# Performance work log

Hardware: AMD Instinct MI355X
Metric: run time of the kernel (lower is better)

## Reference

```python
import jax, jax.numpy as jnp
import numpy as np

N = 100000
E = 1600000
GENE = 512
HID = 128
NCLS = 10
EPS = 1e-5  # BatchNorm1d default eps


def setup_inputs() -> dict:
    key = jax.random.key(0)
    ks = jax.random.split(key, 16)
    def lin(k, fan_in, fan_out):
        return (jax.random.normal(k, (fan_in, fan_out), jnp.float32) / np.sqrt(fan_in)).astype(jnp.float32)
    dims = [(GENE, HID), (HID, 2 * HID), (2 * HID, HID), (HID, HID // 2)]
    inp = {}
    inp["x"] = jax.random.normal(ks[0], (N, GENE), jnp.float32)
    inp["edge_index"] = jax.random.randint(ks[1], (2, E), 0, N)
    for i, (di, do) in enumerate(dims, start=1):
        inp[f"W{i}"] = lin(ks[1 + i], di, do)
        inp[f"b{i}"] = jnp.zeros((do,), jnp.float32)
        inp[f"g{i}"] = jnp.ones((do,), jnp.float32)     # BN gamma
        inp[f"beta{i}"] = jnp.zeros((do,), jnp.float32)  # BN beta
    inp["Wc"] = lin(ks[10], HID // 2, NCLS)
    inp["bc"] = jnp.zeros((NCLS,), jnp.float32)
    return inp


def gcn_conv(h_in, W, b, src, dst, deg_inv_sqrt):
    # PyG GCNConv: transform, then symmetric-normalized aggregation with self-loops
    h = h_in @ W                                   # [N, out]
    norm = (deg_inv_sqrt[src] * deg_inv_sqrt[dst])[:, None]  # [E, 1]
    agg = jnp.zeros_like(h).at[dst].add(h[src] * norm)       # scatter-add over edges
    agg = agg + h * (deg_inv_sqrt ** 2)[:, None]   # self-loop contribution (norm = 1/deg)
    return agg + b


def relu_bn(h, g, beta):
    # forward applies BatchNorm1d(F.relu(h)) in training mode (batch stats, biased var)
    h = jax.nn.relu(h)
    mu = h.mean(axis=0)
    var = h.var(axis=0)
    return (h - mu) * jax.lax.rsqrt(var + EPS) * g + beta


def reference(x, edge_index, W1, b1, g1, beta1, W2, b2, g2, beta2,
              W3, b3, g3, beta3, W4, b4, g4, beta4, Wc, bc):
    src, dst = edge_index[0], edge_index[1]
    # degree after adding self-loops (edge weight 1)
    deg = jnp.zeros((x.shape[0],), x.dtype).at[dst].add(1.0) + 1.0
    dis = jax.lax.rsqrt(deg)
    h = relu_bn(gcn_conv(x, W1, b1, src, dst, dis), g1, beta1)
    h = relu_bn(gcn_conv(h, W2, b2, src, dst, dis), g2, beta2)
    h = relu_bn(gcn_conv(h, W3, b3, src, dst, dis), g3, beta3)
    h = relu_bn(gcn_conv(h, W4, b4, src, dst, dis), g4, beta4)
    return h @ Wc + bc
```

## Files before the change

kernel.cpp:

```cpp
#include <hip/hip_runtime.h>
#include <hip/hip_bf16.h>

#define EPS_BN 1e-5f

using frag8 = __attribute__((ext_vector_type(8))) short;
using f32x4 = __attribute__((ext_vector_type(4))) float;

typedef const __attribute__((address_space(1))) void* gas_ptr;
typedef __attribute__((address_space(3))) void* las_ptr;

__device__ __forceinline__ void async_ld16(const void* g, void* l) {
  __builtin_amdgcn_global_load_lds((gas_ptr)g, (las_ptr)l, 16, 0, 0);
}

__device__ __forceinline__ float bfu2f(unsigned short u) {
  union { unsigned int i; float f; } c;
  c.i = (unsigned int)u << 16;
  return c.f;
}


__global__ void wtrans1_kernel(const float* __restrict__ W1, __hip_bfloat16* __restrict__ T) {
  int i = blockIdx.x * blockDim.x + threadIdx.x;
  if (i < 512 * 128) {
    int k = i / 128, f = i % 128;
    T[f * 512 + k] = __float2bfloat16(W1[i]);
  }
}

__global__ void scan1_kernel(const int* __restrict__ cnt, int* __restrict__ out,
                             int* __restrict__ bsum, float* __restrict__ dis, int n) {
  __shared__ int sdata[1024];
  int tid = threadIdx.x;
  int i = blockIdx.x * 1024 + tid;
  int v = (i < n) ? cnt[i] : 0;
  if (i < n) dis[i] = rsqrtf((float)v + 1.0f);
  sdata[tid] = v;
  __syncthreads();
  for (int off = 1; off < 1024; off <<= 1) {
    int t = (tid >= off) ? sdata[tid - off] : 0;
    __syncthreads();
    sdata[tid] += t;
    __syncthreads();
  }
  if (i < n) out[i] = sdata[tid] - v;
  if (tid == 1023) bsum[blockIdx.x] = sdata[1023];
}

__global__ void scan2_kernel(int* __restrict__ bsum, int nb) {
  __shared__ int sdata[1024];
  int tid = threadIdx.x;
  int v = (tid < nb) ? bsum[tid] : 0;
  sdata[tid] = v;
  __syncthreads();
  for (int off = 1; off < 1024; off <<= 1) {
    int t = (tid >= off) ? sdata[tid - off] : 0;
    __syncthreads();
    sdata[tid] += t;
    __syncthreads();
  }
  if (tid < nb) bsum[tid] = sdata[tid] - v;
}

__global__ void scan3_kernel(int* __restrict__ out, const int* __restrict__ bsum,
                             int n, int E) {
  int i = blockIdx.x * 1024 + threadIdx.x;
  if (i < n) out[i] += bsum[blockIdx.x];
  if (i == 0) out[n] = E;
}

template <int TN, int ASTAGE, int OMODE>
__device__ __forceinline__ void gemm_body(
    const void* __restrict__ Ap, const __hip_bfloat16* __restrict__ Bt,
    __hip_bfloat16* __restrict__ C, const float* __restrict__ bias,
    const float* __restrict__ rowscale,
    const float* __restrict__ statsIn, const float* __restrict__ g,
    const float* __restrict__ beta, float* __restrict__ statsOut, float invN,
    int Nr, int K, int F, int bx, int by) {
  constexpr int WM = (TN == 128) ? 64 : 32;
  constexpr int MI = WM / 16;
  constexpr int BPASS = TN / 64;
  __shared__ __align__(16) __hip_bfloat16 As[2][128 * 32];
  __shared__ __align__(16) __hip_bfloat16 Bs[2][TN * 32];
  __shared__ float sacc[128], sqc[128];
  __shared__ float ssc[256], ssb[256];
  int tid = (int)threadIdx.x;
  int wid = tid >> 6, lane = tid & 63;
  int rowBase = bx * 128;
  int colBase = by * TN;
  int wr, wc;
  if (TN == 128) { wr = (wid >> 1) * 64; wc = (wid & 1) * 64; }
  else           { wr = wid * 32;        wc = 0; }

  f32x4 zero = {0.f, 0.f, 0.f, 0.f};
  f32x4 acc[MI][4];
#pragma unroll
  for (int i = 0; i < MI; ++i)
#pragma unroll
    for (int j = 0; j < 4; ++j) acc[i][j] = zero;

  int lm = lane & 15;
  int k8 = (lane >> 4) * 8;

  int arow[2], alrow[2], akq[2], adst[2];
#pragma unroll
  for (int p = 0; p < 2; ++p) {
    int sidx = p * 256 + tid;
    alrow[p] = sidx >> 2;
    akq[p] = (sidx & 3) * 8;
    int gr = rowBase + alrow[p];
    if (gr >= Nr) gr = Nr - 1;
    arow[p] = gr;
    adst[p] = (p * 256 + wid * 64) * 16;
  }
  int bcol[BPASS], bkq[BPASS], bdst[BPASS];
#pragma unroll
  for (int p = 0; p < BPASS; ++p) {
    int sidx = p * 256 + tid;
    bcol[p] = colBase + (sidx >> 2);
    bkq[p] = (sidx & 3) * 8;
    bdst[p] = (p * 256 + wid * 64) * 16;
  }

  if constexpr (OMODE == 3) {
    if (tid < 128) { sacc[tid] = 0.f; sqc[tid] = 0.f; }
  }
  if constexpr (ASTAGE == 2) {
    for (int k = tid; k < K; k += 256) {
      float mean = statsIn[k] * invN;
      float var = statsIn[256 + k] * invN - mean * mean;
      float sc = g[k] * rsqrtf(var + EPS_BN);
      ssc[k] = sc;
      ssb[k] = beta[k] - mean * sc;
    }
    __syncthreads();
  }

  auto cvt_store_f32 = [&](int p, int buf, float4 a, float4 b2) {
    union { frag8 f; __hip_bfloat16 h[8]; } pk;
    pk.h[0] = __float2bfloat16(a.x);  pk.h[1] = __float2bfloat16(a.y);
    pk.h[2] = __float2bfloat16(a.z);  pk.h[3] = __float2bfloat16(a.w);
    pk.h[4] = __float2bfloat16(b2.x); pk.h[5] = __float2bfloat16(b2.y);
    pk.h[6] = __float2bfloat16(b2.z); pk.h[7] = __float2bfloat16(b2.w);
    *(frag8*)&As[buf][alrow[p] * 32 + akq[p]] = pk.f;
  };
  auto cvt_store_bn = [&](int p, int buf, int kk, ushort4 a, ushort4 b2) {
    union { frag8 f; __hip_bfloat16 h[8]; } pk;
    pk.h[0] = __float2bfloat16(bfu2f(a.x)  * ssc[kk + 0] + ssb[kk + 0]);
    pk.h[1] = __float2bfloat16(bfu2f(a.y)  * ssc[kk + 1] + ssb[kk + 1]);
    pk.h[2] = __float2bfloat16(bfu2f(a.z)  * ssc[kk + 2] + ssb[kk + 2]);
    pk.h[3] = __float2bfloat16(bfu2f(a.w)  * ssc[kk + 3] + ssb[kk + 3]);
    pk.h[4] = __float2bfloat16(bfu2f(b2.x) * ssc[kk + 4] + ssb[kk + 4]);
    pk.h[5] = __float2bfloat16(bfu2f(b2.y) * ssc[kk + 5] + ssb[kk + 5]);
    pk.h[6] = __float2bfloat16(bfu2f(b2.z) * ssc[kk + 6] + ssb[kk + 6]);
    pk.h[7] = __float2bfloat16(bfu2f(b2.w) * ssc[kk + 7] + ssb[kk + 7]);
    *(frag8*)&As[buf][alrow[p] * 32 + akq[p]] = pk.f;
  };

  if constexpr (ASTAGE == 0) {
#pragma unroll
    for (int p = 0; p < 2; ++p)
      async_ld16((const __hip_bfloat16*)Ap + (size_t)arow[p] * K + akq[p],
                 (char*)As[0] + adst[p]);
  } else if constexpr (ASTAGE == 1) {
#pragma unroll
    for (int p = 0; p < 2; ++p) {
      const float* s = (const float*)Ap + (size_t)arow[p] * K + akq[p];
      cvt_store_f32(p, 0, *(const float4*)s, *(const float4*)(s + 4));
    }
  } else {
#pragma unroll
    for (int p = 0; p < 2; ++p) {
      const unsigned short* s = (const unsigned short*)Ap + (size_t)arow[p] * K + akq[p];
      cvt_store_bn(p, 0, akq[p], *(const ushort4*)s, *(const ushort4*)(s + 4));
    }
  }
#pragma unroll
  for (int p = 0; p < BPASS; ++p)
    async_ld16(Bt + (size_t)bcol[p] * K + bkq[p], (char*)Bs[0] + bdst[p]);
  __syncthreads();

  int nt = K >> 5;
  int cur = 0;
  for (int t = 0; t < nt; ++t) {
    int k0n = (t + 1) << 5;
    bool hasNext = (t + 1) < nt;
    float4 pf0[2], pf1[2];
    ushort4 pu0[2], pu1[2];

    if (hasNext) {
      if constexpr (ASTAGE == 0) {
#pragma unroll
        for (int p = 0; p < 2; ++p)
          async_ld16((const __hip_bfloat16*)Ap + (size_t)arow[p] * K + k0n + akq[p],
                     (char*)As[cur ^ 1] + adst[p]);
      } else if constexpr (ASTAGE == 1) {
#pragma unroll
        for (int p = 0; p < 2; ++p) {
          const float* s = (const float*)Ap + (size_t)arow[p] * K + k0n + akq[p];
          pf0[p] = *(const float4*)s;
          pf1[p] = *(const float4*)(s + 4);
        }
      } else {
#pragma unroll
        for (int p = 0; p < 2; ++p) {
          const unsigned short* s =
              (const unsigned short*)Ap + (size_t)arow[p] * K + k0n + akq[p];
          pu0[p] = *(const ushort4*)s;
          pu1[p] = *(const ushort4*)(s + 4);
        }
      }
#pragma unroll
      for (int p = 0; p < BPASS; ++p)
        async_ld16(Bt + (size_t)bcol[p] * K + k0n + bkq[p], (char*)Bs[cur ^ 1] + bdst[p]);
    }

    frag8 af[MI], bfr[4];
#pragma unroll
    for (int i = 0; i < MI; ++i)
      af[i] = *(const frag8*)&As[cur][(wr + i * 16 + lm) * 32 + k8];
#pragma unroll
    for (int j = 0; j < 4; ++j)
      bfr[j] = *(const frag8*)&Bs[cur][(wc + j * 16 + lm) * 32 + k8];
#pragma unroll
    for (int i = 0; i < MI; ++i)
#pragma unroll
      for (int j = 0; j < 4; ++j)
        acc[i][j] = __builtin_amdgcn_mfma_f32_16x16x32_bf16(af[i], bfr[j], acc[i][j], 0, 0, 0);

    if (hasNext) {
      if constexpr (ASTAGE == 1) {
#pragma unroll
        for (int p = 0; p < 2; ++p) cvt_store_f32(p, cur ^ 1, pf0[p], pf1[p]);
      } else if constexpr (ASTAGE == 2) {
#pragma unroll
        for (int p = 0; p < 2; ++p) cvt_store_bn(p, cur ^ 1, k0n + akq[p], pu0[p], pu1[p]);
      }
    }
    __syncthreads();
    cur ^= 1;
  }

  int rquad = (lane >> 4) * 4;
  float s[4] = {0.f, 0.f, 0.f, 0.f}, q[4] = {0.f, 0.f, 0.f, 0.f};
#pragma unroll
  for (int i = 0; i < MI; ++i) {
    int rb = rowBase + wr + i * 16 + rquad;
#pragma unroll
    for (int r = 0; r < 4; ++r) {
      int row = rb + r;
      if (row < Nr) {
        if constexpr (OMODE == 0) {
#pragma unroll
          for (int j = 0; j < 4; ++j) {
            int col = colBase + wc + j * 16 + lm;
            C[(size_t)row * F + col] = __float2bfloat16(acc[i][j][r]);
          }
        } else if constexpr (OMODE == 1) {
          float rs = rowscale[row];
#pragma unroll
          for (int j = 0; j < 4; ++j) {
            int col = colBase + wc + j * 16 + lm;
            C[(size_t)row * F + col] = __float2bfloat16(acc[i][j][r] * rs);
          }
        } else {
#pragma unroll
          for (int j = 0; j < 4; ++j) {
            int col = colBase + wc + j * 16 + lm;
            float v = acc[i][j][r] + bias[col];
            float rl = fmaxf(v, 0.f);
            C[(size_t)row * F + col] = __float2bfloat16(rl);
            s[j] += rl;
            q[j] += rl * rl;
          }
        }
      }
    }
  }

  if constexpr (OMODE == 3) {
#pragma unroll
    for (int j = 0; j < 4; ++j) {
      s[j] += __shfl_xor(s[j], 16, 64); s[j] += __shfl_xor(s[j], 32, 64);
      q[j] += __shfl_xor(q[j], 16, 64); q[j] += __shfl_xor(q[j], 32, 64);
    }
    if (lane < 16) {
#pragma unroll
      for (int j = 0; j < 4; ++j) {
        atomicAdd(&sacc[wc + j * 16 + lane], s[j]);
        atomicAdd(&sqc[wc + j * 16 + lane], q[j]);
      }
    }
    __syncthreads();
    if (tid < 128) {
      atomicAdd(&statsOut[colBase + tid], sacc[tid]);
      atomicAdd(&statsOut[256 + colBase + tid], sqc[tid]);
    }
  }
}

__global__ __launch_bounds__(256) void fat1_kernel(
    const float* __restrict__ x, const __hip_bfloat16* __restrict__ Wt0,
    __hip_bfloat16* __restrict__ T1, int Nn, int G1, int S,
    const int* __restrict__ e_dst, int* __restrict__ cnt, int* __restrict__ rank,
    int E, int CB,
    const float* __restrict__ W2, const float* __restrict__ W3, const float* __restrict__ W4,
    __hip_bfloat16* __restrict__ Tw2, __hip_bfloat16* __restrict__ Tw3,
    __hip_bfloat16* __restrict__ Tw4) {
  int b = (int)blockIdx.x;
  int inter = G1 * S;
  bool isGemm = (b < inter) && (b % S == 0);
  if (isGemm) {
    gemm_body<128, 1, 0>(x, Wt0, T1, nullptr, nullptr, nullptr, nullptr, nullptr,
                         nullptr, 0.f, Nn, 512, 128, b / S, 0);
    return;
  }
  int c = (b < inter) ? (b - b / S - 1) : (b - G1);
  if (c < CB) {
    int e = c * 256 + (int)threadIdx.x;
    if (e < E) rank[e] = atomicAdd(&cnt[e_dst[e]], 1);
  } else {
    int i = (c - CB) * 256 + (int)threadIdx.x;
    const float* W; __hip_bfloat16* T; int K, F, base;
    if (i < 32768)       { W = W2; T = Tw2; K = 128; F = 256; base = 0; }
    else if (i < 65536)  { W = W3; T = Tw3; K = 256; F = 128; base = 32768; }
    else if (i < 73728)  { W = W4; T = Tw4; K = 128; F = 64;  base = 65536; }
    else return;
    int j = i - base;
    int k = j / F, f = j % F;
    T[f * K + k] = __float2bfloat16(W[j]);
  }
}

template <int TN, int ASTAGE, int OMODE>
__global__ __launch_bounds__(256) void mfma_gemm_kernel(
    const void* __restrict__ A, const __hip_bfloat16* __restrict__ Bt,
    __hip_bfloat16* __restrict__ C, const float* __restrict__ bias,
    const float* __restrict__ rowscale, const float* __restrict__ statsIn,
    const float* __restrict__ g, const float* __restrict__ beta,
    float* __restrict__ statsOut, float invN, int Nr, int K, int F) {
  gemm_body<TN, ASTAGE, OMODE>(A, Bt, C, bias, rowscale, statsIn, g, beta, statsOut,
                               invN, Nr, K, F, (int)blockIdx.x, (int)blockIdx.y);
}

__global__ __launch_bounds__(256) void fat2_kernel(
    const int* __restrict__ src, const int* __restrict__ dst,
    const int* __restrict__ rowstart, const int* __restrict__ rank,
    int* __restrict__ csr_src, int E) {
  int e = (int)blockIdx.x * 256 + (int)threadIdx.x;
  if (e < E) csr_src[rowstart[dst[e]] + rank[e]] = src[e];
}

template <int VEC, int AMODE>
__global__ __launch_bounds__(256) void agg_kernel(
    const __hip_bfloat16* __restrict__ Ts, const int* __restrict__ rowstart,
    const int* __restrict__ csr_src, const float* __restrict__ dis,
    const float* __restrict__ bias, void* __restrict__ H,
    float* __restrict__ stats, const float* __restrict__ statsIn,
    const float* __restrict__ g, const float* __restrict__ beta,
    float* __restrict__ sd, float invN, int Nn, int F) {
  __shared__ float lsum[512], lqs[512];
  __shared__ float ssc[128], ssb[128];
  int tid = (int)threadIdx.x;
  int wid4 = tid >> 6;
  int lane = tid & 63;
  int off = lane * VEC;
  const unsigned short* Tu = (const unsigned short*)Ts;

  if constexpr (AMODE == 2) {
    if (tid < F) {
      float mean = statsIn[tid] * invN;
      float var = statsIn[256 + tid] * invN - mean * mean;
      float sc = g[tid] * rsqrtf(var + EPS_BN);
      ssc[tid] = sc;
      ssb[tid] = beta[tid] - mean * sc;
    }
    __syncthreads();
  }

  float bj[VEC];
  float s[VEC], q[VEC];
#pragma unroll
  for (int j = 0; j < VEC; ++j) {
    bj[j] = (AMODE == 1 || AMODE == 3 || AMODE == 4) ? bias[off + j] : 0.f;
    s[j] = 0.f; q[j] = 0.f;
  }

  for (int d = blockIdx.x * 4 + wid4; d < Nn; d += gridDim.x * 4) {
    float dd = dis[d];
    float acc[VEC];
    {
      unsigned short r[VEC];
      if constexpr (VEC == 2) *(ushort2*)r = *(const ushort2*)&Tu[(size_t)d * F + off];
      else                    r[0] = Tu[(size_t)d * F + off];
#pragma unroll
      for (int j = 0; j < VEC; ++j) {
        if constexpr (AMODE == 1) acc[j] = bfu2f(r[j]) * dd;
        else                      acc[j] = bfu2f(r[j]);
      }
    }
    float sdacc = dd;

    int e0 = rowstart[d], e1 = rowstart[d + 1];
    for (int e = e0; e < e1; e += 16) {
      int ee = e + (lane & 15);
      if (ee >= e1) ee = e1 - 1;
      int myidx = csr_src[ee];
      float mydis = 0.f;
      if constexpr (AMODE == 1) mydis = dis[myidx];
      int np = e1 - e;
      if (np > 16) np = 16;
      int sidx[16];
      float sdv[16];
#pragma unroll
      for (int p = 0; p < 16; ++p) {
        sidx[p] = __builtin_amdgcn_readlane(myidx, p);
        if constexpr (AMODE == 1)
          sdv[p] = __uint_as_float(
              (unsigned)__builtin_amdgcn_readlane((int)__float_as_uint(mydis), p));
      }
      unsigned short r[16][VEC];
#pragma unroll
      for (int p = 0; p < 16; ++p) {
        if constexpr (VEC == 2) *(ushort2*)r[p] = *(const ushort2*)&Tu[(size_t)sidx[p] * F + off];
        else                    r[p][0] = Tu[(size_t)sidx[p] * F + off];
      }
#pragma unroll
      for (int p = 0; p < 16; ++p) {
        if (p < np) {
          if constexpr (AMODE == 1) {
#pragma unroll
            for (int j = 0; j < VEC; ++j) acc[j] += bfu2f(r[p][j]) * sdv[p];
            sdacc += sdv[p];
          } else {
#pragma unroll
            for (int j = 0; j < VEC; ++j) acc[j] += bfu2f(r[p][j]);
          }
        }
      }
    }

    if constexpr (AMODE == 2) {
      float sdv = sd[d];
      union { ushort2 u; __hip_bfloat16 h[2]; } pk;
      pk.h[0] = __float2bfloat16(dd * (ssc[off + 0] * acc[0] + ssb[off + 0] * sdv));
      pk.h[1] = __float2bfloat16(dd * (ssc[off + 1] * acc[1] + ssb[off + 1] * sdv));
      *(ushort2*)&((__hip_bfloat16*)H)[(size_t)d * F + off] = pk.u;
    } else {
      float rl[VEC];
#pragma unroll
      for (int j = 0; j < VEC; ++j) {
        float v = acc[j] * dd + bj[j];
        rl[j] = fmaxf(v, 0.f);
        s[j] += rl[j];
        q[j] += rl[j] * rl[j];
      }
      if constexpr (AMODE == 1) {
        union { ushort2 u; __hip_bfloat16 h[2]; } pk;
        pk.h[0] = __float2bfloat16(rl[0] * dd);
        pk.h[1] = __float2bfloat16(rl[1] * dd);
        *(ushort2*)&((__hip_bfloat16*)H)[(size_t)d * F + off] = pk.u;
        if (lane == 0) sd[d] = sdacc;
      } else if constexpr (AMODE == 3) {
        union { ushort2 u; __hip_bfloat16 h[2]; } pk;
        pk.h[0] = __float2bfloat16(rl[0]);
        pk.h[1] = __float2bfloat16(rl[1]);
        *(ushort2*)&((__hip_bfloat16*)H)[(size_t)d * F + off] = pk.u;
      } else {
        ((float*)H)[(size_t)d * F + off] = rl[0];
      }
    }
  }

  if constexpr (AMODE != 2) {
#pragma unroll
    for (int j = 0; j < VEC; ++j) {
      lsum[(lane * VEC + j) * 4 + wid4] = s[j];
      lqs[(lane * VEC + j) * 4 + wid4] = q[j];
    }
    __syncthreads();
    int nc = 64 * VEC;
    for (int c = tid; c < nc; c += 256) {
      float a = lsum[c * 4 + 0] + lsum[c * 4 + 1] + lsum[c * 4 + 2] + lsum[c * 4 + 3];
      float b = lqs[c * 4 + 0] + lqs[c * 4 + 1] + lqs[c * 4 + 2] + lqs[c * 4 + 3];
      atomicAdd(&stats[c], a);
      atomicAdd(&stats[256 + c], b);
    }
  }
}

__global__ __launch_bounds__(256) void bnapply_cls_kernel(
    const float* __restrict__ R4, const float* __restrict__ stats,
    const float* __restrict__ g, const float* __restrict__ beta,
    const float* __restrict__ Wc, const float* __restrict__ bc,
    float* __restrict__ out, int Nn, float invN) {
  __shared__ float ssc[64], ssb[64];
  int tid = (int)threadIdx.x;
  if (tid < 64) {
    float mean = stats[tid] * invN;
    float var = stats[256 + tid] * invN - mean * mean;
    float sc = g[tid] * rsqrtf(var + EPS_BN);
    ssc[tid] = sc;
    ssb[tid] = beta[tid] - mean * sc;
  }
  __syncthreads();
  int gt = blockIdx.x * blockDim.x + tid;
  int wid = gt >> 6;
  int lane = tid & 63;
  if (wid >= Nn) return;
  float v = R4[(size_t)wid * 64 + lane];
  float h = v * ssc[lane] + ssb[lane];
#pragma unroll
  for (int c = 0; c < 10; ++c) {
    float p = h * Wc[lane * 10 + c];
#pragma unroll
    for (int off = 32; off > 0; off >>= 1) p += __shfl_down(p, off, 64);
    if (lane == 0) out[(size_t)wid * 10 + c] = p + bc[c];
  }
}


extern "C" void kernel_launch(void* const* d_in, const int* in_sizes, int n_in,
                              void* d_out, int out_size, void* d_ws, size_t ws_size,
                              hipStream_t stream) {
  (void)n_in; (void)out_size; (void)ws_size;
  const float* x    = (const float*)d_in[0];
  const int*   edge = (const int*)d_in[1];
  const int E  = in_sizes[1] / 2;
  const int Nn = in_sizes[0] / 512;
  const int* e_src = edge;
  const int* e_dst = edge + E;

  const float* W[4]  = {(const float*)d_in[2],  (const float*)d_in[6],
                        (const float*)d_in[10], (const float*)d_in[14]};
  const float* bv[4] = {(const float*)d_in[3],  (const float*)d_in[7],
                        (const float*)d_in[11], (const float*)d_in[15]};
  const float* gv[4] = {(const float*)d_in[4],  (const float*)d_in[8],
                        (const float*)d_in[12], (const float*)d_in[16]};
  const float* bt[4] = {(const float*)d_in[5],  (const float*)d_in[9],
                        (const float*)d_in[13], (const float*)d_in[17]};
  const float* Wc = (const float*)d_in[18];
  const float* bc = (const float*)d_in[19];
  float* out = (float*)d_out;

  const float invN = 1.0f / (float)Nn;

  char* p = (char*)d_ws;
  auto alloc = [&](size_t bytes) -> void* {
    void* r = (void*)p;
    p += (bytes + 255) & ~(size_t)255;
    return r;
  };
  int*   cnt      = (int*)alloc((size_t)Nn * 4);
  float* stats    = (float*)alloc(2048 * 4);
  size_t zeroBytes = (size_t)(((size_t)Nn * 4 + 255) & ~(size_t)255) + 2048 * 4;
  int*   rowstart = (int*)alloc((size_t)(Nn + 1) * 4);
  int*   bsum     = (int*)alloc(1024 * 4);
  float* dis      = (float*)alloc((size_t)Nn * 4);
  float* sd       = (float*)alloc((size_t)Nn * 4);
  int*   rank     = (int*)alloc((size_t)E * 4);
  int*   csr_src  = (int*)alloc((size_t)E * 4);
  __hip_bfloat16* Wt0 = (__hip_bfloat16*)alloc(512 * 128 * 2);
  __hip_bfloat16* Wt1 = (__hip_bfloat16*)alloc(128 * 256 * 2);
  __hip_bfloat16* Wt2 = (__hip_bfloat16*)alloc(256 * 128 * 2);
  __hip_bfloat16* Wt3 = (__hip_bfloat16*)alloc(128 * 64 * 2);
  __hip_bfloat16* Ts1 = (__hip_bfloat16*)alloc((size_t)Nn * 128 * 2);
  __hip_bfloat16* R1  = (__hip_bfloat16*)alloc((size_t)Nn * 128 * 2);
  __hip_bfloat16* Tb2 = (__hip_bfloat16*)alloc((size_t)Nn * 128 * 2);
  __hip_bfloat16* R2  = (__hip_bfloat16*)alloc((size_t)Nn * 256 * 2);
  __hip_bfloat16* Ts3 = (__hip_bfloat16*)alloc((size_t)Nn * 128 * 2);
  __hip_bfloat16* R3  = (__hip_bfloat16*)alloc((size_t)Nn * 128 * 2);
  __hip_bfloat16* Ts4 = (__hip_bfloat16*)alloc((size_t)Nn * 64 * 2);
  float*          R4  = (float*)alloc((size_t)Nn * 64 * 4);

  hipMemsetAsync(cnt, 0, zeroBytes, stream);

  wtrans1_kernel<<<(512 * 128 + 255) / 256, 256, 0, stream>>>(W[0], Wt0);

  const int gx = (Nn + 127) / 128;
  const int CB = (E + 255) / 256;
  const int WB = (73728 + 255) / 256;
  const int S  = 1 + (CB + WB) / gx;
  fat1_kernel<<<gx + CB + WB, 256, 0, stream>>>(
      x, Wt0, Ts1, Nn, gx, S, e_dst, cnt, rank, E, CB,
      W[1], W[2], W[3], Wt1, Wt2, Wt3);

  int nb = (Nn + 1023) / 1024;
  scan1_kernel<<<nb, 1024, 0, stream>>>(cnt, rowstart, bsum, dis, Nn);
  scan2_kernel<<<1, 1024, 0, stream>>>(bsum, nb);
  scan3_kernel<<<nb, 1024, 0, stream>>>(rowstart, bsum, Nn, E);

  fat2_kernel<<<CB, 256, 0, stream>>>(e_src, e_dst, rowstart, rank, csr_src, E);

  const int AGG_BLOCKS = 2048;

  agg_kernel<2, 1><<<AGG_BLOCKS, 256, 0, stream>>>(
      Ts1, rowstart, csr_src, dis, bv[0], R1, stats, nullptr, nullptr, nullptr,
      sd, invN, Nn, 128);
  agg_kernel<2, 2><<<AGG_BLOCKS, 256, 0, stream>>>(
      R1, rowstart, csr_src, dis, nullptr, Tb2, nullptr, stats, gv[0], bt[0],
      sd, invN, Nn, 128);
  {
    dim3 g(gx, 2);
    mfma_gemm_kernel<128, 0, 3><<<g, 256, 0, stream>>>(
        Tb2, Wt1, R2, bv[1], nullptr, nullptr, nullptr, nullptr, stats + 512, invN,
        Nn, 128, 256);
  }
  {
    dim3 g(gx, 1);
    mfma_gemm_kernel<128, 2, 1><<<g, 256, 0, stream>>>(
        R2, Wt2, Ts3, nullptr, dis, stats + 512, gv[1], bt[1], nullptr, invN,
        Nn, 256, 128);
  }
  agg_kernel<2, 3><<<AGG_BLOCKS, 256, 0, stream>>>(
      Ts3, rowstart, csr_src, dis, bv[2], R3, stats + 1024, nullptr, nullptr, nullptr,
      nullptr, invN, Nn, 128);
  {
    dim3 g(gx, 1);
    mfma_gemm_kernel<64, 2, 1><<<g, 256, 0, stream>>>(
        R3, Wt3, Ts4, nullptr, dis, stats + 1024, gv[2], bt[2], nullptr, invN,
        Nn, 128, 64);
  }
  agg_kernel<1, 4><<<AGG_BLOCKS, 256, 0, stream>>>(
      Ts4, rowstart, csr_src, dis, bv[3], R4, stats + 1536, nullptr, nullptr, nullptr,
      nullptr, invN, Nn, 64);
  int clsBlocks = (Nn * 64 + 255) / 256;
  bnapply_cls_kernel<<<clsBlocks, 256, 0, stream>>>(R4, stats + 1536, gv[3], bt[3],
                                                    Wc, bc, out, Nn, invN);
}
```

Measured before the change: 946.0 us.

## Split wavefront into two half-waves gathering separate edges with 8-byte loads

For the 128-feature aggregation path, each wavefront now splits into two 32-lane halves. Each half gathers a different neighbor row with 4 bf16 values per lane (ushort4) instead of all 64 lanes reading 2 values of the same row. The partial sums are combined with a cross-half shuffle, and the self-loop term and epilogue are handled by the lower half only. This halves the number of gather instructions per edge and widens each memory access, at the cost of an extra shuffle and idle upper lanes in the epilogue.

```diff
diff --git a/kernel.cpp b/kernel.cpp
--- a/kernel.cpp
+++ b/kernel.cpp
@@ -364,7 +364,6 @@
   int tid = (int)threadIdx.x;
   int wid4 = tid >> 6;
   int lane = tid & 63;
-  int off = lane * VEC;
   const unsigned short* Tu = (const unsigned short*)Ts;
 
   if constexpr (AMODE == 2) {
@@ -378,101 +377,160 @@
     __syncthreads();
   }
 
-  float bj[VEC];
-  float s[VEC], q[VEC];
-#pragma unroll
-  for (int j = 0; j < VEC; ++j) {
-    bj[j] = (AMODE == 1 || AMODE == 3 || AMODE == 4) ? bias[off + j] : 0.f;
-    s[j] = 0.f; q[j] = 0.f;
-  }
-
-  for (int d = blockIdx.x * 4 + wid4; d < Nn; d += gridDim.x * 4) {
-    float dd = dis[d];
-    float acc[VEC];
-    {
-      unsigned short r[VEC];
-      if constexpr (VEC == 2) *(ushort2*)r = *(const ushort2*)&Tu[(size_t)d * F + off];
-      else                    r[0] = Tu[(size_t)d * F + off];
-#pragma unroll
-      for (int j = 0; j < VEC; ++j) {
-        if constexpr (AMODE == 1) acc[j] = bfu2f(r[j]) * dd;
-        else                      acc[j] = bfu2f(r[j]);
-      }
-    }
-    float sdacc = dd;
-
-    int e0 = rowstart[d], e1 = rowstart[d + 1];
-    for (int e = e0; e < e1; e += 16) {
-      int ee = e + (lane & 15);
-      if (ee >= e1) ee = e1 - 1;
-      int myidx = csr_src[ee];
-      float mydis = 0.f;
-      if constexpr (AMODE == 1) mydis = dis[myidx];
-      int np = e1 - e;
-      if (np > 16) np = 16;
-      int sidx[16];
-      float sdv[16];
-#pragma unroll
-      for (int p = 0; p < 16; ++p) {
-        sidx[p] = __builtin_amdgcn_readlane(myidx, p);
-        if constexpr (AMODE == 1)
-          sdv[p] = __uint_as_float(
-              (unsigned)__builtin_amdgcn_readlane((int)__float_as_uint(mydis), p));
-      }
-      unsigned short r[16][VEC];
-#pragma unroll
-      for (int p = 0; p < 16; ++p) {
-        if constexpr (VEC == 2) *(ushort2*)r[p] = *(const ushort2*)&Tu[(size_t)sidx[p] * F + off];
-        else                    r[p][0] = Tu[(size_t)sidx[p] * F + off];
-      }
-#pragma unroll
-      for (int p = 0; p < 16; ++p) {
-        if (p < np) {
+  if constexpr (VEC == 2) {
+    int fb = (lane & 31) * 4;
+    int rsel = lane >> 5;
+    float bj4[4], s4[4], q4[4];
+#pragma unroll
+    for (int j = 0; j < 4; ++j) {
+      bj4[j] = (AMODE == 1 || AMODE == 3) ? bias[fb + j] : 0.f;
+      s4[j] = 0.f; q4[j] = 0.f;
+    }
+
+    for (int d = blockIdx.x * 4 + wid4; d < Nn; d += gridDim.x * 4) {
+      float dd = dis[d];
+      float acc[4] = {0.f, 0.f, 0.f, 0.f};
+      float sdacc = dd;
+
+      int e0 = rowstart[d], e1 = rowstart[d + 1];
+      for (int e = e0; e < e1; e += 16) {
+        int ee = e + (lane & 15);
+        if (ee >= e1) ee = e1 - 1;
+        int myidx = csr_src[ee];
+        float mydis = 0.f;
+        if constexpr (AMODE == 1) mydis = dis[myidx];
+        int np = e1 - e;
+        if (np > 16) np = 16;
+        int sidx[16];
+        float sdv[16];
+#pragma unroll
+        for (int p = 0; p < 16; ++p) {
+          sidx[p] = __builtin_amdgcn_readlane(myidx, p);
+          if constexpr (AMODE == 1)
+            sdv[p] = __uint_as_float(
+                (unsigned)__builtin_amdgcn_readlane((int)__float_as_uint(mydis), p));
+        }
+#pragma unroll
+        for (int p = 0; p < 8; ++p) {
+          int ridx = rsel ? sidx[2 * p + 1] : sidx[2 * p];
+          union { ushort4 u; unsigned short h[4]; } rv;
+          rv.u = *(const ushort4*)&Tu[(size_t)ridx * 128 + fb];
+          bool valid = (2 * p + rsel) < np;
           if constexpr (AMODE == 1) {
-#pragma unroll
-            for (int j = 0; j < VEC; ++j) acc[j] += bfu2f(r[p][j]) * sdv[p];
-            sdacc += sdv[p];
+            float w = valid ? (rsel ? sdv[2 * p + 1] : sdv[2 * p]) : 0.f;
+#pragma unroll
+            for (int j = 0; j < 4; ++j) acc[j] += bfu2f(rv.h[j]) * w;
           } else {
 #pragma unroll
-            for (int j = 0; j < VEC; ++j) acc[j] += bfu2f(r[p][j]);
+            for (int j = 0; j < 4; ++j) acc[j] += valid ? bfu2f(rv.h[j]) : 0.f;
           }
         }
-      }
-    }
-
-    if constexpr (AMODE == 2) {
-      float sdv = sd[d];
-      union { ushort2 u; __hip_bfloat16 h[2]; } pk;
-      pk.h[0] = __float2bfloat16(dd * (ssc[off + 0] * acc[0] + ssb[off + 0] * sdv));
-      pk.h[1] = __float2bfloat16(dd * (ssc[off + 1] * acc[1] + ssb[off + 1] * sdv));
-      *(ushort2*)&((__hip_bfloat16*)H)[(size_t)d * F + off] = pk.u;
-    } else {
-      float rl[VEC];
-#pragma unroll
-      for (int j = 0; j < VEC; ++j) {
-        float v = acc[j] * dd + bj[j];
-        rl[j] = fmaxf(v, 0.f);
-        s[j] += rl[j];
-        q[j] += rl[j] * rl[j];
-      }
-      if constexpr (AMODE == 1) {
-        union { ushort2 u; __hip_bfloat16 h[2]; } pk;
-        pk.h[0] = __float2bfloat16(rl[0] * dd);
-        pk.h[1] = __float2bfloat16(rl[1] * dd);
-        *(ushort2*)&((__hip_bfloat16*)H)[(size_t)d * F + off] = pk.u;
-        if (lane == 0) sd[d] = sdacc;
-      } else if constexpr (AMODE == 3) {
-        union { ushort2 u; __hip_bfloat16 h[2]; } pk;
-        pk.h[0] = __float2bfloat16(rl[0]);
-        pk.h[1] = __float2bfloat16(rl[1]);
-        *(ushort2*)&((__hip_bfloat16*)H)[(size_t)d * F + off] = pk.u;
-      } else {
-        ((float*)H)[(size_t)d * F + off] = rl[0];
-      }
-    }
-  }
-
-  if constexpr (AMODE != 2) {
+        if constexpr (AMODE == 1) {
+#pragma unroll
+          for (int p = 0; p < 16; ++p)
+            if (p < np) sdacc += sdv[p];
+        }
+      }
+
+#pragma unroll
+      for (int j = 0; j < 4; ++j) acc[j] += __shfl_xor(acc[j], 32, 64);
+
+      if (lane < 32) {
+        union { ushort4 u; unsigned short h[4]; } sv;
+        sv.u = *(const ushort4*)&Tu[(size_t)d * 128 + fb];
+#pragma unroll
+        for (int j = 0; j < 4; ++j)
+          acc[j] += (AMODE == 1) ? bfu2f(sv.h[j]) * dd : bfu2f(sv.h[j]);
+
+        if constexpr (AMODE == 2) {
+          float sdv_ = sd[d];
+          union { ushort4 u; __hip_bfloat16 h[4]; } pk;
+#pragma unroll
+          for (int j = 0; j < 4; ++j)
+            pk.h[j] = __float2bfloat16(dd * (ssc[fb + j] * acc[j] + ssb[fb + j] * sdv_));
+          *(ushort4*)&((__hip_bfloat16*)H)[(size_t)d * 128 + fb] = pk.u;
+        } else {
+          float rl[4];
+#pragma unroll
+          for (int j = 0; j < 4; ++j) {
+            float v = acc[j] * dd + bj4[j];
+            rl[j] = fmaxf(v, 0.f);
+            s4[j] += rl[j];
+            q4[j] += rl[j] * rl[j];
+          }
+          union { ushort4 u; __hip_bfloat16 h[4]; } pk;
+          if constexpr (AMODE == 1) {
+#pragma unroll
+            for (int j = 0; j < 4; ++j) pk.h[j] = __float2bfloat16(rl[j] * dd);
+            *(ushort4*)&((__hip_bfloat16*)H)[(size_t)d * 128 + fb] = pk.u;
+            if (lane == 0) sd[d] = sdacc;
+          } else {
+#pragma unroll
+            for (int j = 0; j < 4; ++j) pk.h[j] = __float2bfloat16(rl[j]);
+            *(ushort4*)&((__hip_bfloat16*)H)[(size_t)d * 128 + fb] = pk.u;
+          }
+        }
+      }
+    }
+
+    if constexpr (AMODE != 2) {
+      if (lane < 32) {
+#pragma unroll
+        for (int j = 0; j < 4; ++j) {
+          lsum[(fb + j) * 4 + wid4] = s4[j];
+          lqs[(fb + j) * 4 + wid4] = q4[j];
+        }
+      }
+      __syncthreads();
+      for (int c = tid; c < 128; c += 256) {
+        float a = lsum[c * 4 + 0] + lsum[c * 4 + 1] + lsum[c * 4 + 2] + lsum[c * 4 + 3];
+        float b = lqs[c * 4 + 0] + lqs[c * 4 + 1] + lqs[c * 4 + 2] + lqs[c * 4 + 3];
+        atomicAdd(&stats[c], a);
+        atomicAdd(&stats[256 + c], b);
+      }
+    }
+  } else {
+    int off = lane * VEC;
+    float bj[VEC], s[VEC], q[VEC];
+#pragma unroll
+    for (int j = 0; j < VEC; ++j) {
+      bj[j] = (AMODE == 1 || AMODE == 3 || AMODE == 4) ? bias[off + j] : 0.f;
+      s[j] = 0.f; q[j] = 0.f;
+    }
+
+    for (int d = blockIdx.x * 4 + wid4; d < Nn; d += gridDim.x * 4) {
+      float dd = dis[d];
+      float acc[VEC];
+      {
+        unsigned short r0 = Tu[(size_t)d * F + off];
+        acc[0] = bfu2f(r0);
+      }
+
+      int e0 = rowstart[d], e1 = rowstart[d + 1];
+      for (int e = e0; e < e1; e += 16) {
+        int ee = e + (lane & 15);
+        if (ee >= e1) ee = e1 - 1;
+        int myidx = csr_src[ee];
+        int np = e1 - e;
+        if (np > 16) np = 16;
+        int sidx[16];
+#pragma unroll
+        for (int p = 0; p < 16; ++p) sidx[p] = __builtin_amdgcn_readlane(myidx, p);
+        unsigned short r[16];
+#pragma unroll
+        for (int p = 0; p < 16; ++p) r[p] = Tu[(size_t)sidx[p] * F + off];
+#pragma unroll
+        for (int p = 0; p < 16; ++p)
+          if (p < np) acc[0] += bfu2f(r[p]);
+      }
+
+      float v = acc[0] * dd + bj[0];
+      float rl = fmaxf(v, 0.f);
+      s[0] += rl;
+      q[0] += rl * rl;
+      ((float*)H)[(size_t)d * F + off] = rl;
+    }
+
 #pragma unroll
     for (int j = 0; j < VEC; ++j) {
       lsum[(lane * VEC + j) * 4 + wid4] = s[j];
```

Measured after the change: 1.043 ms. +10.2%, slower.
